# Kernel optimization log

Hardware: AMD Instinct MI355X
Metric: run time of the kernel (lower is better)

## Reference

```python
import jax, jax.numpy as jnp
import numpy as np

ANCHORS = [[(0.0156,0.0203),(0.025,0.0469),(0.0516,0.0359)],
           [(0.0469,0.0953),(0.0969,0.0703),(0.0922,0.1859)],
           [(0.1813,0.1406),(0.2438,0.3094),(0.5828,0.5094)]]
IMG = 640.0; NC = 80; NA = 3
LAM_NOOBJ = 1.0; LAM_OBJ = 1.0; LAM_CLS = 1.0; LAM_BOX = 5.0
ALPHA = 0.25; GAMMA = 2.0
GRIDS = [(80, 80), (40, 40), (20, 20)]


def _bce(x, t):
    # numerically-stable BCEWithLogits, reduction='none'
    return jnp.maximum(x, 0.0) - x * t + jnp.log1p(jnp.exp(-jnp.abs(x)))


def _focal(x, t):
    p = jax.nn.sigmoid(x)
    pt = p * t + (1.0 - p) * (1.0 - t)
    at = ALPHA * t + (1.0 - ALPHA) * (1.0 - t)
    return at * (1.0 - pt) ** GAMMA


def setup_inputs() -> dict:
    key = jax.random.key(0)
    ks = jax.random.split(key, 6)
    p0 = jax.random.normal(ks[0], (16, 255, 80, 80), jnp.float32)
    p1 = jax.random.normal(ks[1], (16, 255, 40, 40), jnp.float32)
    p2 = jax.random.normal(ks[2], (16, 255, 20, 20), jnp.float32)
    cxy = jax.random.uniform(ks[3], (16, 32, 2), jnp.float32, 32.0, 608.0)
    wh = jax.random.uniform(ks[4], (16, 32, 2), jnp.float32, 8.0, 256.0)
    target_boxes = jnp.clip(jnp.concatenate([cxy - wh / 2, cxy + wh / 2], -1), 0.0, IMG)
    target_labels = jax.random.randint(ks[5], (16, 32), 0, NC)
    return {"p0": p0, "p1": p1, "p2": p2, "target_boxes": target_boxes, "target_labels": target_labels}


def _loss(preds, boxes, labels):
    anchors = jnp.asarray(ANCHORS, jnp.float32)  # (3, 3, 2)
    B, N = labels.shape
    x1, y1, x2, y2 = boxes[..., 0], boxes[..., 1], boxes[..., 2], boxes[..., 3]
    bw = jnp.clip((x2 - x1) / IMG, 1e-6, 1.0)
    bh = jnp.clip((y2 - y1) / IMG, 1e-6, 1.0)
    # shape IoU against all 9 anchors -> top-1 (scale, anchor) per GT
    aw = anchors.reshape(-1, 2)  # (9, 2)
    inter = jnp.minimum(bw[..., None], aw[:, 0]) * jnp.minimum(bh[..., None], aw[:, 1])
    iou = inter / (bw[..., None] * bh[..., None] + aw[:, 0] * aw[:, 1] - inter + 1e-9)  # (B,N,9)
    best = jnp.argmax(iou, -1)
    scale_idx = best // NA
    anchor_idx = best % NA
    valid = (labels >= 0) & (labels < NC)
    cx = jnp.clip((x1 + x2) * 0.5 / IMG, 0.0, 1.0 - 1e-6)
    cy = jnp.clip((y1 + y2) * 0.5 / IMG, 0.0, 1.0 - 1e-6)
    oh = jax.nn.one_hot(labels, NC, dtype=jnp.float32)  # (B,N,NC)
    tb = jnp.stack([cx, cy, bw, bh], -1)  # (B,N,4) normalized cxcywh
    obj_loss = 0.0; cls_loss = 0.0; box_loss = 0.0; npos = 0.0
    for s, (pred, (h, w)) in enumerate(zip(preds, GRIDS)):
        pred = pred.reshape(B, NA, 5 + NC, h, w)
        gx = cx * w; gy = cy * h
        gi = jnp.clip(jnp.floor(gx), 0, w - 1).astype(jnp.int32)
        gj = jnp.clip(jnp.floor(gy), 0, h - 1).astype(jnp.int32)
        fx = gx - gi; fy = gy - gj
        base = valid & (scale_idx == s)
        ones = jnp.ones_like(fx, bool)
        cand = [(0, 0, ones), (-1, 0, fx < 0.5), (1, 0, fx >= 0.5), (0, -1, fy < 0.5), (0, 1, fy >= 0.5)]
        Ms, GIs, GJs = [], [], []
        for di, dj, keep in cand:
            ngi = gi + di; ngj = gj + dj
            inb = (ngi >= 0) & (ngi < w) & (ngj >= 0) & (ngj < h)
            Ms.append(base & keep & inb)
            GIs.append(jnp.clip(ngi, 0, w - 1))
            GJs.append(jnp.clip(ngj, 0, h - 1))
        M = jnp.stack(Ms); GI = jnp.stack(GIs); GJ = jnp.stack(GJs)  # (5,B,N)
        bidx = jnp.arange(B, dtype=jnp.int32)[None, :, None]
        aidx = jnp.broadcast_to(anchor_idx.astype(jnp.int32)[None], M.shape)
        flat = ((bidx * NA + aidx) * h + GJ) * w + GI  # (5,B,N) index into (B,NA,h,w)
        ncell = B * NA * h * w
        safe = jnp.where(M, flat, ncell)  # invalid -> dummy row
        pos = jax.lax.stop_gradient(
            jnp.zeros(ncell + 1).at[safe].max(M.astype(jnp.float32))[:ncell].reshape(B, NA, h, w))
        cls_t = jax.lax.stop_gradient(
            jnp.zeros((ncell + 1, NC)).at[safe].max(
                jnp.broadcast_to(oh[None], (5, B, N, NC)) * M[..., None].astype(jnp.float32)
            )[:ncell].reshape(B, NA, h, w, NC))
        box_t = jnp.zeros((ncell + 1, 4)).at[safe].set(
            jnp.broadcast_to(tb[None], (5, B, N, 4)))[:ncell].reshape(B, NA, h, w, 4)
        # decode (YOLOv5 parameterization), normalized coords
        sig = jax.nn.sigmoid
        pxy = 2.0 * sig(pred[:, :, :2]) - 0.5  # (B,NA,2,h,w)
        gxr = jnp.arange(w, dtype=jnp.float32)[None, None, None, :]
        gyr = jnp.arange(h, dtype=jnp.float32)[None, None, :, None]
        pcx = (gxr + pxy[:, :, 0]) / w
        pcy = (gyr + pxy[:, :, 1]) / h
        pwh = (2.0 * sig(pred[:, :, 2:4])) ** 2 * anchors[s][None, :, :, None, None]
        pw = pwh[:, :, 0]; ph = pwh[:, :, 1]
        tcx = box_t[..., 0]; tcy = box_t[..., 1]; tw = box_t[..., 2]; th = box_t[..., 3]
        px1, px2 = pcx - pw / 2, pcx + pw / 2; py1, py2 = pcy - ph / 2, pcy + ph / 2
        tx1, tx2 = tcx - tw / 2, tcx + tw / 2; ty1, ty2 = tcy - th / 2, tcy + th / 2
        iw = jnp.maximum(jnp.minimum(px2, tx2) - jnp.maximum(px1, tx1), 0.0)
        ih = jnp.maximum(jnp.minimum(py2, ty2) - jnp.maximum(py1, ty1), 0.0)
        it = iw * ih
        un = pw * ph + tw * th - it + 1e-9
        iouc = it / un
        enc = (jnp.maximum(px2, tx2) - jnp.minimum(px1, tx1)) * (jnp.maximum(py2, ty2) - jnp.minimum(py1, ty1)) + 1e-9
        giou = iouc - (enc - un) / enc
        l1 = jnp.abs(pcx - tcx) + jnp.abs(pcy - tcy) + jnp.abs(pw - tw) + jnp.abs(ph - th)
        box_loss = box_loss + (((1.0 - giou) + l1) * pos).sum()
        pcls = jnp.transpose(pred[:, :, 5:], (0, 1, 3, 4, 2))  # (B,NA,h,w,NC)
        cls_loss = cls_loss + (_bce(pcls, cls_t).sum(-1) * pos).sum()
        pobj = pred[:, :, 4]
        fb = _focal(pobj, pos) * _bce(pobj, pos)
        obj_loss = obj_loss + (fb * jnp.where(pos > 0, LAM_OBJ, LAM_NOOBJ)).mean()
        npos = npos + pos.sum()
    d = jnp.maximum(npos, 1.0)
    return obj_loss + LAM_CLS * cls_loss / d + LAM_BOX * box_loss / d


def reference(p0, p1, p2, target_boxes, target_labels):
    return _loss([p0, p1, p2], target_boxes, target_labels)
```

## Files before the change

kernel.cpp:

```cpp
#include <hip/hip_runtime.h>
#include <math.h>


#define IMGF 640.0f
#define NCLS 80
#define NAK 3
#define NB 16
#define NT 32
#define H0 80
#define H1 40
#define H2 20
#define NCELL0 (NB * NAK * H0 * H0)
#define NCELL1 (NB * NAK * H1 * H1)
#define NCELL2 (NB * NAK * H2 * H2)
#define NCELL_TOTAL (NCELL0 + NCELL1 + NCELL2)
#define MAXPOS 1536
#define NDENSE (NCELL_TOTAL / 4)
#define NDBLK ((NDENSE + 255) / 256)
#define POS_BLOCKS (MAXPOS * 64 / 256)
#define HSIZE 4096

__device__ __constant__ float c_anchors[9][2] = {
    {0.0156f, 0.0203f}, {0.025f, 0.0469f}, {0.0516f, 0.0359f},
    {0.0469f, 0.0953f}, {0.0969f, 0.0703f}, {0.0922f, 0.1859f},
    {0.1813f, 0.1406f}, {0.2438f, 0.3094f}, {0.5828f, 0.5094f}};

__device__ inline float sgm(float x) { return 1.f / (1.f + expf(-x)); }
__device__ inline float bcef(float x, float t) {
    return fmaxf(x, 0.f) - x * t + log1pf(expf(-fabsf(x)));
}
__device__ inline float focal_bce(float x, float t) {
    float p = sgm(x);
    float pt = p * t + (1.f - p) * (1.f - t);
    float at = 0.25f * t + 0.75f * (1.f - t);
    float omp = 1.f - pt;
    return at * omp * omp * bcef(x, t);
}

__global__ __launch_bounds__(512) void assign_kernel(
    const float* __restrict__ boxes, const int* __restrict__ labels,
    int4* __restrict__ list, int* __restrict__ countg, int* __restrict__ done) {
    __shared__ int hkey[HSIZE];
    __shared__ int hord[HSIZE];
    __shared__ unsigned htm[HSIZE];
    __shared__ int lcount;
    for (int i = threadIdx.x; i < HSIZE; i += 512) {
        hkey[i] = -1;
        hord[i] = -1;
        htm[i] = 0u;
    }
    if (threadIdx.x == 0) lcount = 0;
    __syncthreads();

    int t = threadIdx.x;
    int b = t >> 5;
    int n = t & 31;
    int lab = labels[t];
    if (lab >= 0 && lab < NCLS) {
        float x1 = boxes[4 * t + 0], y1 = boxes[4 * t + 1];
        float x2 = boxes[4 * t + 2], y2 = boxes[4 * t + 3];
        float bw = fminf(fmaxf((x2 - x1) / IMGF, 1e-6f), 1.0f);
        float bh = fminf(fmaxf((y2 - y1) / IMGF, 1e-6f), 1.0f);
        float area = bw * bh;
        float best = -1.0f;
        int bestk = 0;
#pragma unroll
        for (int k = 0; k < 9; k++) {
            float aw = c_anchors[k][0], ah = c_anchors[k][1];
            float inter = fminf(bw, aw) * fminf(bh, ah);
            float iou = inter / (area + aw * ah - inter + 1e-9f);
            if (iou > best) { best = iou; bestk = k; }
        }
        int s = bestk / 3, a = bestk - 3 * s;
        float cx = fminf(fmaxf((x1 + x2) * 0.5f / IMGF, 0.f), 1.f - 1e-6f);
        float cy = fminf(fmaxf((y1 + y2) * 0.5f / IMGF, 0.f), 1.f - 1e-6f);
        int hw = (s == 0) ? H0 : ((s == 1) ? H1 : H2);
        int basecell = (s == 0) ? 0 : ((s == 1) ? NCELL0 : (NCELL0 + NCELL1));
        float gx = cx * (float)hw, gy = cy * (float)hw;
        int gi = min(max((int)floorf(gx), 0), hw - 1);
        int gj = min(max((int)floorf(gy), 0), hw - 1);
        float fx = gx - (float)gi, fy = gy - (float)gj;
        const int dis[5] = {0, -1, 1, 0, 0};
        const int djs[5] = {0, 0, 0, -1, 1};
        bool keep[5];
        keep[0] = true;
        keep[1] = (fx < 0.5f);
        keep[2] = (fx >= 0.5f);
        keep[3] = (fy < 0.5f);
        keep[4] = (fy >= 0.5f);
#pragma unroll
        for (int c = 0; c < 5; c++) {
            if (!keep[c]) continue;
            int ngi = gi + dis[c], ngj = gj + djs[c];
            if (ngi < 0 || ngi >= hw || ngj < 0 || ngj >= hw) continue;
            int cell = basecell + ((b * NAK + a) * hw + ngj) * hw + ngi;
            unsigned h = ((unsigned)cell * 2654435761u) >> 20;
            while (true) {
                int old = atomicCAS(&hkey[h], -1, cell);
                if (old == -1 || old == cell) break;
                h = (h + 1) & (HSIZE - 1);
            }
            atomicMax(&hord[h], c * (NB * NT) + t);
            atomicOr(&htm[h], 1u << n);
        }
    }
    __syncthreads();
    for (int i = threadIdx.x; i < HSIZE; i += 512) {
        if (hkey[i] >= 0) {
            int p = atomicAdd(&lcount, 1);
            list[p] = make_int4(hkey[i], hord[i], (int)htm[i], 0);
        }
    }
    __syncthreads();
    if (threadIdx.x == 0) {
        *countg = lcount;
        *done = 0;
    }
}

template <int HWC>
__device__ inline float obj4(const float* __restrict__ p, int cis, float inv) {
    int q = cis / HWC;
    int off = cis - q * HWC;
    const float4 v =
        *reinterpret_cast<const float4*>(p + ((size_t)q * 85 + 4) * HWC + off);
    return (focal_bce(v.x, 0.f) + focal_bce(v.y, 0.f) + focal_bce(v.z, 0.f) +
            focal_bce(v.w, 0.f)) *
           inv;
}

__global__ __launch_bounds__(256) void dense_kernel(
    const float* __restrict__ p0, const float* __restrict__ p1,
    const float* __restrict__ p2, float* __restrict__ dpart) {
    int i = blockIdx.x * 256 + threadIdx.x;
    float obj = 0.f;
    if (i < NDENSE) {
        int c4 = i * 4;
        if (c4 < NCELL0)
            obj = obj4<H0 * H0>(p0, c4, 1.f / (float)NCELL0);
        else if (c4 < NCELL0 + NCELL1)
            obj = obj4<H1 * H1>(p1, c4 - NCELL0, 1.f / (float)NCELL1);
        else
            obj = obj4<H2 * H2>(p2, c4 - NCELL0 - NCELL1, 1.f / (float)NCELL2);
    }
#pragma unroll
    for (int off = 32; off > 0; off >>= 1) obj += __shfl_down(obj, off, 64);
    __shared__ float red[4];
    if ((threadIdx.x & 63) == 0) red[threadIdx.x >> 6] = obj;
    __syncthreads();
    if (threadIdx.x == 0)
        dpart[blockIdx.x] = red[0] + red[1] + red[2] + red[3];
}

__global__ __launch_bounds__(256) void pos_kernel(
    const float* __restrict__ p0, const float* __restrict__ p1,
    const float* __restrict__ p2, const float* __restrict__ boxes,
    const int* __restrict__ labels, const int4* __restrict__ list,
    const int* __restrict__ countg, int* __restrict__ done,
    const float* __restrict__ dpart, float* __restrict__ ppart,
    float* __restrict__ out) {
    int cnt = *countg;
    int w = (blockIdx.x * 256 + threadIdx.x) >> 6;
    int lane = threadIdx.x & 63;
    if (w < cnt) {
        int4 rec = list[w];
        int idx = rec.x;
        unsigned tm = (unsigned)rec.z;
        const float* p;
        int hw, s, base;
        float inv;
        if (idx < NCELL0) {
            p = p0; hw = H0; s = 0; base = 0; inv = 1.f / (float)NCELL0;
        } else if (idx < NCELL0 + NCELL1) {
            p = p1; hw = H1; s = 1; base = NCELL0; inv = 1.f / (float)NCELL1;
        } else {
            p = p2; hw = H2; s = 2; base = NCELL0 + NCELL1;
            inv = 1.f / (float)NCELL2;
        }
        int cell = idx - base;
        int x = cell % hw;
        int r = cell / hw;
        int y = r % hw;
        r /= hw;
        int a = r % NAK;
        int b = r / NAK;
        size_t HW = (size_t)hw * hw;
        const float* pc =
            p + (size_t)(b * 255 + a * 85) * HW + (size_t)y * hw + x;
        float cl = 0.f;
#pragma unroll
        for (int rep = 0; rep < 2; rep++) {
            int c = lane + 64 * rep;
            if (c < NCLS) {
                float tt = 0.f;
                unsigned tmp = tm;
                while (tmp) {
                    int n = __ffs(tmp) - 1;
                    tmp &= tmp - 1;
                    if (labels[(b << 5) + n] == c) tt = 1.f;
                }
                cl += bcef(pc[(size_t)(5 + c) * HW], tt);
            }
        }
#pragma unroll
        for (int off = 32; off > 0; off >>= 1) cl += __shfl_down(cl, off, 64);
        if (lane == 0) {
            float pobj = pc[4 * HW];
            float objc = (focal_bce(pobj, 1.f) - focal_bce(pobj, 0.f)) * inv;
            int wn = rec.y & (NB * NT - 1);
            float bx1 = boxes[4 * wn + 0], by1 = boxes[4 * wn + 1];
            float bx2 = boxes[4 * wn + 2], by2 = boxes[4 * wn + 3];
            float tw = fminf(fmaxf((bx2 - bx1) / IMGF, 1e-6f), 1.f);
            float th = fminf(fmaxf((by2 - by1) / IMGF, 1e-6f), 1.f);
            float tcx =
                fminf(fmaxf((bx1 + bx2) * 0.5f / IMGF, 0.f), 1.f - 1e-6f);
            float tcy =
                fminf(fmaxf((by1 + by2) * 0.5f / IMGF, 0.f), 1.f - 1e-6f);
            float l0 = pc[0], l1 = pc[HW], l2 = pc[2 * HW], l3 = pc[3 * HW];
            float pcx = ((float)x + 2.f * sgm(l0) - 0.5f) / (float)hw;
            float pcy = ((float)y + 2.f * sgm(l1) - 0.5f) / (float)hw;
            float sw = 2.f * sgm(l2), sh = 2.f * sgm(l3);
            float pw = sw * sw * c_anchors[s * 3 + a][0];
            float ph = sh * sh * c_anchors[s * 3 + a][1];
            float px1 = pcx - pw * 0.5f, px2 = pcx + pw * 0.5f;
            float py1 = pcy - ph * 0.5f, py2 = pcy + ph * 0.5f;
            float tx1 = tcx - tw * 0.5f, tx2 = tcx + tw * 0.5f;
            float ty1 = tcy - th * 0.5f, ty2 = tcy + th * 0.5f;
            float iw = fmaxf(fminf(px2, tx2) - fmaxf(px1, tx1), 0.f);
            float ih = fmaxf(fminf(py2, ty2) - fmaxf(py1, ty1), 0.f);
            float it = iw * ih;
            float un = pw * ph + tw * th - it + 1e-9f;
            float iou = it / un;
            float enc = (fmaxf(px2, tx2) - fminf(px1, tx1)) *
                            (fmaxf(py2, ty2) - fminf(py1, ty1)) +
                        1e-9f;
            float giou = iou - (enc - un) / enc;
            float l1l = fabsf(pcx - tcx) + fabsf(pcy - tcy) + fabsf(pw - tw) +
                        fabsf(ph - th);
            ppart[3 * w] = cl;
            ppart[3 * w + 1] = 1.f - giou + l1l;
            ppart[3 * w + 2] = objc;
        }
    }
    __shared__ int amLast;
    __syncthreads();
    if (threadIdx.x == 0) {
        __threadfence();
        int old = atomicAdd(done, 1);
        amLast = (old == POS_BLOCKS - 1) ? 1 : 0;
    }
    __syncthreads();
    if (amLast) {
        __threadfence();
        float obj = 0.f, cls = 0.f, box = 0.f;
        for (int i = threadIdx.x; i < NDBLK; i += 256) obj += dpart[i];
        for (int i = threadIdx.x; i < cnt; i += 256) {
            cls += ppart[3 * i];
            box += ppart[3 * i + 1];
            obj += ppart[3 * i + 2];
        }
#pragma unroll
        for (int off = 32; off > 0; off >>= 1) {
            obj += __shfl_down(obj, off, 64);
            cls += __shfl_down(cls, off, 64);
            box += __shfl_down(box, off, 64);
        }
        __shared__ float red[4][3];
        int wv = threadIdx.x >> 6;
        if ((threadIdx.x & 63) == 0) {
            red[wv][0] = obj;
            red[wv][1] = cls;
            red[wv][2] = box;
        }
        __syncthreads();
        if (threadIdx.x == 0) {
            float o = red[0][0] + red[1][0] + red[2][0] + red[3][0];
            float c = red[0][1] + red[1][1] + red[2][1] + red[3][1];
            float bx = red[0][2] + red[1][2] + red[2][2] + red[3][2];
            float d = fmaxf((float)cnt, 1.f);
            out[0] = o + (c + 5.f * bx) / d;
        }
    }
}

extern "C" void kernel_launch(void* const* d_in, const int* in_sizes, int n_in,
                              void* d_out, int out_size, void* d_ws,
                              size_t ws_size, hipStream_t stream) {
    const float* p0 = (const float*)d_in[0];
    const float* p1 = (const float*)d_in[1];
    const float* p2 = (const float*)d_in[2];
    const float* boxes = (const float*)d_in[3];
    const int* labels = (const int*)d_in[4];
    float* out = (float*)d_out;

    char* ws = (char*)d_ws;
    int4* list = (int4*)ws;
    size_t off = (size_t)MAXPOS * 16;
    int* countg = (int*)(ws + off);
    int* done = (int*)(ws + off + 4);
    off += 16;
    float* dpart = (float*)(ws + off);
    off += (size_t)((NDBLK + 3) / 4 * 4) * 4;
    float* ppart = (float*)(ws + off);

    assign_kernel<<<1, 512, 0, stream>>>(boxes, labels, list, countg, done);
    dense_kernel<<<NDBLK, 256, 0, stream>>>(p0, p1, p2, dpart);
    pos_kernel<<<POS_BLOCKS, 256, 0, stream>>>(p0, p1, p2, boxes, labels, list,
                                               countg, done, dpart, ppart, out);
}
```

Measured before the change: 31.19 us.

## Fuse assign, dense and positive kernels into one persistent kernel with flag sync

Merges the three launches into a single 384-block kernel. Block 0 builds the target-assignment hash list and then publishes it through a global ready flag. Every block runs a grid-stride dense objectness reduction, then spins on the flag before processing positive cells, and the last block does the final reduction. This removes two kernel launch gaps and lets the assignment overlap the dense pass. In exchange it depends on all blocks being co-resident to avoid deadlock, carries 48KB of shared memory in every block, and relies on resetting the flag for the next call.

```diff
diff --git a/kernel.cpp b/kernel.cpp
--- a/kernel.cpp
+++ b/kernel.cpp
@@ -16,9 +16,9 @@
 #define NCELL_TOTAL (NCELL0 + NCELL1 + NCELL2)
 #define MAXPOS 1536
 #define NDENSE (NCELL_TOTAL / 4)
-#define NDBLK ((NDENSE + 255) / 256)
-#define POS_BLOCKS (MAXPOS * 64 / 256)
+#define NBLOCKS 384
 #define HSIZE 4096
+#define READY_MAGIC 0x5A17C0DEu
 
 __device__ __constant__ float c_anchors[9][2] = {
     {0.0156f, 0.0203f}, {0.025f, 0.0469f}, {0.0516f, 0.0359f},
@@ -35,87 +35,6 @@
     float at = 0.25f * t + 0.75f * (1.f - t);
     float omp = 1.f - pt;
     return at * omp * omp * bcef(x, t);
-}
-
-__global__ __launch_bounds__(512) void assign_kernel(
-    const float* __restrict__ boxes, const int* __restrict__ labels,
-    int4* __restrict__ list, int* __restrict__ countg, int* __restrict__ done) {
-    __shared__ int hkey[HSIZE];
-    __shared__ int hord[HSIZE];
-    __shared__ unsigned htm[HSIZE];
-    __shared__ int lcount;
-    for (int i = threadIdx.x; i < HSIZE; i += 512) {
-        hkey[i] = -1;
-        hord[i] = -1;
-        htm[i] = 0u;
-    }
-    if (threadIdx.x == 0) lcount = 0;
-    __syncthreads();
-
-    int t = threadIdx.x;
-    int b = t >> 5;
-    int n = t & 31;
-    int lab = labels[t];
-    if (lab >= 0 && lab < NCLS) {
-        float x1 = boxes[4 * t + 0], y1 = boxes[4 * t + 1];
-        float x2 = boxes[4 * t + 2], y2 = boxes[4 * t + 3];
-        float bw = fminf(fmaxf((x2 - x1) / IMGF, 1e-6f), 1.0f);
-        float bh = fminf(fmaxf((y2 - y1) / IMGF, 1e-6f), 1.0f);
-        float area = bw * bh;
-        float best = -1.0f;
-        int bestk = 0;
-#pragma unroll
-        for (int k = 0; k < 9; k++) {
-            float aw = c_anchors[k][0], ah = c_anchors[k][1];
-            float inter = fminf(bw, aw) * fminf(bh, ah);
-            float iou = inter / (area + aw * ah - inter + 1e-9f);
-            if (iou > best) { best = iou; bestk = k; }
-        }
-        int s = bestk / 3, a = bestk - 3 * s;
-        float cx = fminf(fmaxf((x1 + x2) * 0.5f / IMGF, 0.f), 1.f - 1e-6f);
-        float cy = fminf(fmaxf((y1 + y2) * 0.5f / IMGF, 0.f), 1.f - 1e-6f);
-        int hw = (s == 0) ? H0 : ((s == 1) ? H1 : H2);
-        int basecell = (s == 0) ? 0 : ((s == 1) ? NCELL0 : (NCELL0 + NCELL1));
-        float gx = cx * (float)hw, gy = cy * (float)hw;
-        int gi = min(max((int)floorf(gx), 0), hw - 1);
-        int gj = min(max((int)floorf(gy), 0), hw - 1);
-        float fx = gx - (float)gi, fy = gy - (float)gj;
-        const int dis[5] = {0, -1, 1, 0, 0};
-        const int djs[5] = {0, 0, 0, -1, 1};
-        bool keep[5];
-        keep[0] = true;
-        keep[1] = (fx < 0.5f);
-        keep[2] = (fx >= 0.5f);
-        keep[3] = (fy < 0.5f);
-        keep[4] = (fy >= 0.5f);
-#pragma unroll
-        for (int c = 0; c < 5; c++) {
-            if (!keep[c]) continue;
-            int ngi = gi + dis[c], ngj = gj + djs[c];
-            if (ngi < 0 || ngi >= hw || ngj < 0 || ngj >= hw) continue;
-            int cell = basecell + ((b * NAK + a) * hw + ngj) * hw + ngi;
-            unsigned h = ((unsigned)cell * 2654435761u) >> 20;
-            while (true) {
-                int old = atomicCAS(&hkey[h], -1, cell);
-                if (old == -1 || old == cell) break;
-                h = (h + 1) & (HSIZE - 1);
-            }
-            atomicMax(&hord[h], c * (NB * NT) + t);
-            atomicOr(&htm[h], 1u << n);
-        }
-    }
-    __syncthreads();
-    for (int i = threadIdx.x; i < HSIZE; i += 512) {
-        if (hkey[i] >= 0) {
-            int p = atomicAdd(&lcount, 1);
-            list[p] = make_int4(hkey[i], hord[i], (int)htm[i], 0);
-        }
-    }
-    __syncthreads();
-    if (threadIdx.x == 0) {
-        *countg = lcount;
-        *done = 0;
-    }
 }
 
 template <int HWC>
@@ -129,38 +48,132 @@
            inv;
 }
 
-__global__ __launch_bounds__(256) void dense_kernel(
+__global__ __launch_bounds__(256, 2) void yolo_fused(
     const float* __restrict__ p0, const float* __restrict__ p1,
-    const float* __restrict__ p2, float* __restrict__ dpart) {
-    int i = blockIdx.x * 256 + threadIdx.x;
+    const float* __restrict__ p2, const float* __restrict__ boxes,
+    const int* __restrict__ labels, int4* __restrict__ list,
+    int* __restrict__ countg, unsigned* __restrict__ flag,
+    int* __restrict__ done, float* __restrict__ dpart,
+    float* __restrict__ ppart, float* __restrict__ out) {
+    __shared__ int hkey[HSIZE];
+    __shared__ int hord[HSIZE];
+    __shared__ unsigned htm[HSIZE];
+    __shared__ int lcount;
+    __shared__ float redd[4];
+    __shared__ float redf[4][3];
+    __shared__ int amLast;
+
+    if (blockIdx.x == 0) {
+        for (int i = threadIdx.x; i < HSIZE; i += 256) {
+            hkey[i] = -1;
+            hord[i] = -1;
+            htm[i] = 0u;
+        }
+        if (threadIdx.x == 0) lcount = 0;
+        __syncthreads();
+        for (int half = 0; half < 2; half++) {
+            int t = threadIdx.x + (half << 8);
+            int b = t >> 5;
+            int n = t & 31;
+            int lab = labels[t];
+            if (lab >= 0 && lab < NCLS) {
+                float x1 = boxes[4 * t + 0], y1 = boxes[4 * t + 1];
+                float x2 = boxes[4 * t + 2], y2 = boxes[4 * t + 3];
+                float bw = fminf(fmaxf((x2 - x1) / IMGF, 1e-6f), 1.0f);
+                float bh = fminf(fmaxf((y2 - y1) / IMGF, 1e-6f), 1.0f);
+                float area = bw * bh;
+                float best = -1.0f;
+                int bestk = 0;
+#pragma unroll
+                for (int k = 0; k < 9; k++) {
+                    float aw = c_anchors[k][0], ah = c_anchors[k][1];
+                    float inter = fminf(bw, aw) * fminf(bh, ah);
+                    float iou = inter / (area + aw * ah - inter + 1e-9f);
+                    if (iou > best) { best = iou; bestk = k; }
+                }
+                int s = bestk / 3, a = bestk - 3 * s;
+                float cx =
+                    fminf(fmaxf((x1 + x2) * 0.5f / IMGF, 0.f), 1.f - 1e-6f);
+                float cy =
+                    fminf(fmaxf((y1 + y2) * 0.5f / IMGF, 0.f), 1.f - 1e-6f);
+                int hw = (s == 0) ? H0 : ((s == 1) ? H1 : H2);
+                int basecell =
+                    (s == 0) ? 0 : ((s == 1) ? NCELL0 : (NCELL0 + NCELL1));
+                float gx = cx * (float)hw, gy = cy * (float)hw;
+                int gi = min(max((int)floorf(gx), 0), hw - 1);
+                int gj = min(max((int)floorf(gy), 0), hw - 1);
+                float fx = gx - (float)gi, fy = gy - (float)gj;
+                const int dis[5] = {0, -1, 1, 0, 0};
+                const int djs[5] = {0, 0, 0, -1, 1};
+                bool keep[5];
+                keep[0] = true;
+                keep[1] = (fx < 0.5f);
+                keep[2] = (fx >= 0.5f);
+                keep[3] = (fy < 0.5f);
+                keep[4] = (fy >= 0.5f);
+#pragma unroll
+                for (int c = 0; c < 5; c++) {
+                    if (!keep[c]) continue;
+                    int ngi = gi + dis[c], ngj = gj + djs[c];
+                    if (ngi < 0 || ngi >= hw || ngj < 0 || ngj >= hw) continue;
+                    int cell = basecell + ((b * NAK + a) * hw + ngj) * hw + ngi;
+                    unsigned h = ((unsigned)cell * 2654435761u) >> 20;
+                    while (true) {
+                        int old = atomicCAS(&hkey[h], -1, cell);
+                        if (old == -1 || old == cell) break;
+                        h = (h + 1) & (HSIZE - 1);
+                    }
+                    atomicMax(&hord[h], c * (NB * NT) + t);
+                    atomicOr(&htm[h], 1u << n);
+                }
+            }
+        }
+        __syncthreads();
+        for (int i = threadIdx.x; i < HSIZE; i += 256) {
+            if (hkey[i] >= 0) {
+                int p = atomicAdd(&lcount, 1);
+                list[p] = make_int4(hkey[i], hord[i], (int)htm[i], 0);
+            }
+        }
+        __syncthreads();
+        if (threadIdx.x == 0) {
+            *countg = lcount;
+            *done = 0;
+            __threadfence();
+            __hip_atomic_store(flag, READY_MAGIC, __ATOMIC_RELAXED,
+                               __HIP_MEMORY_SCOPE_AGENT);
+        }
+    }
+
     float obj = 0.f;
-    if (i < NDENSE) {
+    for (int i = blockIdx.x * 256 + threadIdx.x; i < NDENSE;
+         i += NBLOCKS * 256) {
         int c4 = i * 4;
         if (c4 < NCELL0)
-            obj = obj4<H0 * H0>(p0, c4, 1.f / (float)NCELL0);
+            obj += obj4<H0 * H0>(p0, c4, 1.f / (float)NCELL0);
         else if (c4 < NCELL0 + NCELL1)
-            obj = obj4<H1 * H1>(p1, c4 - NCELL0, 1.f / (float)NCELL1);
+            obj += obj4<H1 * H1>(p1, c4 - NCELL0, 1.f / (float)NCELL1);
         else
-            obj = obj4<H2 * H2>(p2, c4 - NCELL0 - NCELL1, 1.f / (float)NCELL2);
+            obj +=
+                obj4<H2 * H2>(p2, c4 - NCELL0 - NCELL1, 1.f / (float)NCELL2);
     }
 #pragma unroll
     for (int off = 32; off > 0; off >>= 1) obj += __shfl_down(obj, off, 64);
-    __shared__ float red[4];
-    if ((threadIdx.x & 63) == 0) red[threadIdx.x >> 6] = obj;
+    if ((threadIdx.x & 63) == 0) redd[threadIdx.x >> 6] = obj;
     __syncthreads();
     if (threadIdx.x == 0)
-        dpart[blockIdx.x] = red[0] + red[1] + red[2] + red[3];
-}
-
-__global__ __launch_bounds__(256) void pos_kernel(
-    const float* __restrict__ p0, const float* __restrict__ p1,
-    const float* __restrict__ p2, const float* __restrict__ boxes,
-    const int* __restrict__ labels, const int4* __restrict__ list,
-    const int* __restrict__ countg, int* __restrict__ done,
-    const float* __restrict__ dpart, float* __restrict__ ppart,
-    float* __restrict__ out) {
+        dpart[blockIdx.x] = redd[0] + redd[1] + redd[2] + redd[3];
+
+    if (threadIdx.x == 0) {
+        while (__hip_atomic_load(flag, __ATOMIC_RELAXED,
+                                 __HIP_MEMORY_SCOPE_AGENT) != READY_MAGIC)
+            __builtin_amdgcn_s_sleep(1);
+    }
+    __syncthreads();
+    __threadfence();
     int cnt = *countg;
-    int w = (blockIdx.x * 256 + threadIdx.x) >> 6;
+
+    int w = blockIdx.x * 4 + (threadIdx.x >> 6);
     int lane = threadIdx.x & 63;
     if (w < cnt) {
         int4 rec = list[w];
@@ -242,43 +255,42 @@
             ppart[3 * w + 2] = objc;
         }
     }
-    __shared__ int amLast;
+
     __syncthreads();
     if (threadIdx.x == 0) {
         __threadfence();
-        int old = atomicAdd(done, 1);
-        amLast = (old == POS_BLOCKS - 1) ? 1 : 0;
+        amLast = (atomicAdd(done, 1) == NBLOCKS - 1) ? 1 : 0;
     }
     __syncthreads();
     if (amLast) {
         __threadfence();
-        float obj = 0.f, cls = 0.f, box = 0.f;
-        for (int i = threadIdx.x; i < NDBLK; i += 256) obj += dpart[i];
+        float o = 0.f, cls = 0.f, box = 0.f;
+        for (int i = threadIdx.x; i < NBLOCKS; i += 256) o += dpart[i];
         for (int i = threadIdx.x; i < cnt; i += 256) {
             cls += ppart[3 * i];
             box += ppart[3 * i + 1];
-            obj += ppart[3 * i + 2];
+            o += ppart[3 * i + 2];
         }
 #pragma unroll
         for (int off = 32; off > 0; off >>= 1) {
-            obj += __shfl_down(obj, off, 64);
+            o += __shfl_down(o, off, 64);
             cls += __shfl_down(cls, off, 64);
             box += __shfl_down(box, off, 64);
         }
-        __shared__ float red[4][3];
         int wv = threadIdx.x >> 6;
         if ((threadIdx.x & 63) == 0) {
-            red[wv][0] = obj;
-            red[wv][1] = cls;
-            red[wv][2] = box;
+            redf[wv][0] = o;
+            redf[wv][1] = cls;
+            redf[wv][2] = box;
         }
         __syncthreads();
         if (threadIdx.x == 0) {
-            float o = red[0][0] + red[1][0] + red[2][0] + red[3][0];
-            float c = red[0][1] + red[1][1] + red[2][1] + red[3][1];
-            float bx = red[0][2] + red[1][2] + red[2][2] + red[3][2];
+            float oo = redf[0][0] + redf[1][0] + redf[2][0] + redf[3][0];
+            float cc = redf[0][1] + redf[1][1] + redf[2][1] + redf[3][1];
+            float bb = redf[0][2] + redf[1][2] + redf[2][2] + redf[3][2];
             float d = fmaxf((float)cnt, 1.f);
-            out[0] = o + (c + 5.f * bx) / d;
+            out[0] = oo + (cc + 5.f * bb) / d;
+            *flag = 0u;
         }
     }
 }
@@ -297,14 +309,14 @@
     int4* list = (int4*)ws;
     size_t off = (size_t)MAXPOS * 16;
     int* countg = (int*)(ws + off);
-    int* done = (int*)(ws + off + 4);
+    unsigned* flag = (unsigned*)(ws + off + 4);
+    int* done = (int*)(ws + off + 8);
     off += 16;
     float* dpart = (float*)(ws + off);
-    off += (size_t)((NDBLK + 3) / 4 * 4) * 4;
+    off += (size_t)NBLOCKS * 4;
     float* ppart = (float*)(ws + off);
 
-    assign_kernel<<<1, 512, 0, stream>>>(boxes, labels, list, countg, done);
-    dense_kernel<<<NDBLK, 256, 0, stream>>>(p0, p1, p2, dpart);
-    pos_kernel<<<POS_BLOCKS, 256, 0, stream>>>(p0, p1, p2, boxes, labels, list,
-                                               countg, done, dpart, ppart, out);
-}
+    yolo_fused<<<NBLOCKS, 256, 0, stream>>>(p0, p1, p2, boxes, labels, list,
+                                            countg, flag, done, dpart, ppart,
+                                            out);
+}
```

After: 52.67 us. 1.69x slower.

## Fuse assignment, dense objectness and positive-cell loss into one kernel

Applied to the files above, without the earlier changes.

Replaces the three-kernel pipeline (single-block assign, dense objectness, positive-cell kernel with a last-block reduction) with one 384-block kernel plus a tiny finalize kernel. Every block redundantly rebuilds the GT-to-cell hash table in shared memory, issuing its two float4 objectness loads before doing so to hide latency, then handles the positive cells whose key modulo the block count equals its block id. This removes the serial single-block assign launch and the global list handoff. In exchange every block repeats the 512-target assignment and shared-memory atomics, and the hash table shrinks to 2048 entries.

```diff
diff --git a/kernel.cpp b/kernel.cpp
--- a/kernel.cpp
+++ b/kernel.cpp
@@ -16,9 +16,8 @@
 #define NCELL_TOTAL (NCELL0 + NCELL1 + NCELL2)
 #define MAXPOS 1536
 #define NDENSE (NCELL_TOTAL / 4)
-#define NDBLK ((NDENSE + 255) / 256)
-#define POS_BLOCKS (MAXPOS * 64 / 256)
-#define HSIZE 4096
+#define NBLKF 384
+#define HSIZE 2048
 
 __device__ __constant__ float c_anchors[9][2] = {
     {0.0156f, 0.0203f}, {0.025f, 0.0469f}, {0.0516f, 0.0359f},
@@ -37,135 +36,143 @@
     return at * omp * omp * bcef(x, t);
 }
 
-__global__ __launch_bounds__(512) void assign_kernel(
-    const float* __restrict__ boxes, const int* __restrict__ labels,
-    int4* __restrict__ list, int* __restrict__ countg, int* __restrict__ done) {
+__device__ inline const float* objaddr(const float* __restrict__ p0,
+                                       const float* __restrict__ p1,
+                                       const float* __restrict__ p2, int c4,
+                                       float& inv) {
+    if (c4 < NCELL0) {
+        inv = 1.f / (float)NCELL0;
+        int q = c4 / (H0 * H0);
+        return p0 + ((size_t)q * 85 + 4) * (H0 * H0) + (c4 - q * (H0 * H0));
+    } else if (c4 < NCELL0 + NCELL1) {
+        inv = 1.f / (float)NCELL1;
+        c4 -= NCELL0;
+        int q = c4 / (H1 * H1);
+        return p1 + ((size_t)q * 85 + 4) * (H1 * H1) + (c4 - q * (H1 * H1));
+    } else {
+        inv = 1.f / (float)NCELL2;
+        c4 -= NCELL0 + NCELL1;
+        int q = c4 / (H2 * H2);
+        return p2 + ((size_t)q * 85 + 4) * (H2 * H2) + (c4 - q * (H2 * H2));
+    }
+}
+
+__device__ inline float fb4_zero(float4 v) {
+    return focal_bce(v.x, 0.f) + focal_bce(v.y, 0.f) + focal_bce(v.z, 0.f) +
+           focal_bce(v.w, 0.f);
+}
+
+__global__ __launch_bounds__(256) void yolo_main(
+    const float* __restrict__ p0, const float* __restrict__ p1,
+    const float* __restrict__ p2, const float* __restrict__ boxes,
+    const int* __restrict__ labels, float* __restrict__ dpart) {
     __shared__ int hkey[HSIZE];
     __shared__ int hord[HSIZE];
     __shared__ unsigned htm[HSIZE];
-    __shared__ int lcount;
-    for (int i = threadIdx.x; i < HSIZE; i += 512) {
+    __shared__ int qslots[MAXPOS];
+    __shared__ int qn;
+    __shared__ float redf[4][4];
+
+    const int tid = threadIdx.x;
+    const int bid = blockIdx.x;
+
+    int i0 = bid * 256 + tid;
+    int i1 = i0 + NBLKF * 256;
+    float inv0, inv1 = 0.f;
+    const float4 v0 =
+        *reinterpret_cast<const float4*>(objaddr(p0, p1, p2, i0 * 4, inv0));
+    float4 v1 = make_float4(0.f, 0.f, 0.f, 0.f);
+    const bool has1 = (i1 < NDENSE);
+    if (has1)
+        v1 = *reinterpret_cast<const float4*>(
+            objaddr(p0, p1, p2, i1 * 4, inv1));
+
+    for (int i = tid; i < HSIZE; i += 256) {
         hkey[i] = -1;
         hord[i] = -1;
         htm[i] = 0u;
     }
-    if (threadIdx.x == 0) lcount = 0;
-    __syncthreads();
-
-    int t = threadIdx.x;
-    int b = t >> 5;
-    int n = t & 31;
-    int lab = labels[t];
-    if (lab >= 0 && lab < NCLS) {
-        float x1 = boxes[4 * t + 0], y1 = boxes[4 * t + 1];
-        float x2 = boxes[4 * t + 2], y2 = boxes[4 * t + 3];
-        float bw = fminf(fmaxf((x2 - x1) / IMGF, 1e-6f), 1.0f);
-        float bh = fminf(fmaxf((y2 - y1) / IMGF, 1e-6f), 1.0f);
-        float area = bw * bh;
-        float best = -1.0f;
-        int bestk = 0;
-#pragma unroll
-        for (int k = 0; k < 9; k++) {
-            float aw = c_anchors[k][0], ah = c_anchors[k][1];
-            float inter = fminf(bw, aw) * fminf(bh, ah);
-            float iou = inter / (area + aw * ah - inter + 1e-9f);
-            if (iou > best) { best = iou; bestk = k; }
-        }
-        int s = bestk / 3, a = bestk - 3 * s;
-        float cx = fminf(fmaxf((x1 + x2) * 0.5f / IMGF, 0.f), 1.f - 1e-6f);
-        float cy = fminf(fmaxf((y1 + y2) * 0.5f / IMGF, 0.f), 1.f - 1e-6f);
-        int hw = (s == 0) ? H0 : ((s == 1) ? H1 : H2);
-        int basecell = (s == 0) ? 0 : ((s == 1) ? NCELL0 : (NCELL0 + NCELL1));
-        float gx = cx * (float)hw, gy = cy * (float)hw;
-        int gi = min(max((int)floorf(gx), 0), hw - 1);
-        int gj = min(max((int)floorf(gy), 0), hw - 1);
-        float fx = gx - (float)gi, fy = gy - (float)gj;
-        const int dis[5] = {0, -1, 1, 0, 0};
-        const int djs[5] = {0, 0, 0, -1, 1};
-        bool keep[5];
-        keep[0] = true;
-        keep[1] = (fx < 0.5f);
-        keep[2] = (fx >= 0.5f);
-        keep[3] = (fy < 0.5f);
-        keep[4] = (fy >= 0.5f);
-#pragma unroll
-        for (int c = 0; c < 5; c++) {
-            if (!keep[c]) continue;
-            int ngi = gi + dis[c], ngj = gj + djs[c];
-            if (ngi < 0 || ngi >= hw || ngj < 0 || ngj >= hw) continue;
-            int cell = basecell + ((b * NAK + a) * hw + ngj) * hw + ngi;
-            unsigned h = ((unsigned)cell * 2654435761u) >> 20;
-            while (true) {
-                int old = atomicCAS(&hkey[h], -1, cell);
-                if (old == -1 || old == cell) break;
-                h = (h + 1) & (HSIZE - 1);
+    if (tid == 0) qn = 0;
+    __syncthreads();
+    for (int half = 0; half < 2; half++) {
+        int t = tid + (half << 8);
+        int b = t >> 5;
+        int n = t & 31;
+        int lab = labels[t];
+        if (lab >= 0 && lab < NCLS) {
+            float x1 = boxes[4 * t + 0], y1 = boxes[4 * t + 1];
+            float x2 = boxes[4 * t + 2], y2 = boxes[4 * t + 3];
+            float bw = fminf(fmaxf((x2 - x1) / IMGF, 1e-6f), 1.0f);
+            float bh = fminf(fmaxf((y2 - y1) / IMGF, 1e-6f), 1.0f);
+            float area = bw * bh;
+            float best = -1.0f;
+            int bestk = 0;
+#pragma unroll
+            for (int k = 0; k < 9; k++) {
+                float aw = c_anchors[k][0], ah = c_anchors[k][1];
+                float inter = fminf(bw, aw) * fminf(bh, ah);
+                float iou = inter / (area + aw * ah - inter + 1e-9f);
+                if (iou > best) { best = iou; bestk = k; }
             }
-            atomicMax(&hord[h], c * (NB * NT) + t);
-            atomicOr(&htm[h], 1u << n);
-        }
-    }
-    __syncthreads();
-    for (int i = threadIdx.x; i < HSIZE; i += 512) {
-        if (hkey[i] >= 0) {
-            int p = atomicAdd(&lcount, 1);
-            list[p] = make_int4(hkey[i], hord[i], (int)htm[i], 0);
-        }
-    }
-    __syncthreads();
-    if (threadIdx.x == 0) {
-        *countg = lcount;
-        *done = 0;
-    }
-}
-
-template <int HWC>
-__device__ inline float obj4(const float* __restrict__ p, int cis, float inv) {
-    int q = cis / HWC;
-    int off = cis - q * HWC;
-    const float4 v =
-        *reinterpret_cast<const float4*>(p + ((size_t)q * 85 + 4) * HWC + off);
-    return (focal_bce(v.x, 0.f) + focal_bce(v.y, 0.f) + focal_bce(v.z, 0.f) +
-            focal_bce(v.w, 0.f)) *
-           inv;
-}
-
-__global__ __launch_bounds__(256) void dense_kernel(
-    const float* __restrict__ p0, const float* __restrict__ p1,
-    const float* __restrict__ p2, float* __restrict__ dpart) {
-    int i = blockIdx.x * 256 + threadIdx.x;
-    float obj = 0.f;
-    if (i < NDENSE) {
-        int c4 = i * 4;
-        if (c4 < NCELL0)
-            obj = obj4<H0 * H0>(p0, c4, 1.f / (float)NCELL0);
-        else if (c4 < NCELL0 + NCELL1)
-            obj = obj4<H1 * H1>(p1, c4 - NCELL0, 1.f / (float)NCELL1);
-        else
-            obj = obj4<H2 * H2>(p2, c4 - NCELL0 - NCELL1, 1.f / (float)NCELL2);
-    }
-#pragma unroll
-    for (int off = 32; off > 0; off >>= 1) obj += __shfl_down(obj, off, 64);
-    __shared__ float red[4];
-    if ((threadIdx.x & 63) == 0) red[threadIdx.x >> 6] = obj;
-    __syncthreads();
-    if (threadIdx.x == 0)
-        dpart[blockIdx.x] = red[0] + red[1] + red[2] + red[3];
-}
-
-__global__ __launch_bounds__(256) void pos_kernel(
-    const float* __restrict__ p0, const float* __restrict__ p1,
-    const float* __restrict__ p2, const float* __restrict__ boxes,
-    const int* __restrict__ labels, const int4* __restrict__ list,
-    const int* __restrict__ countg, int* __restrict__ done,
-    const float* __restrict__ dpart, float* __restrict__ ppart,
-    float* __restrict__ out) {
-    int cnt = *countg;
-    int w = (blockIdx.x * 256 + threadIdx.x) >> 6;
-    int lane = threadIdx.x & 63;
-    if (w < cnt) {
-        int4 rec = list[w];
-        int idx = rec.x;
-        unsigned tm = (unsigned)rec.z;
+            int s = bestk / 3, a = bestk - 3 * s;
+            float cx = fminf(fmaxf((x1 + x2) * 0.5f / IMGF, 0.f), 1.f - 1e-6f);
+            float cy = fminf(fmaxf((y1 + y2) * 0.5f / IMGF, 0.f), 1.f - 1e-6f);
+            int hw = (s == 0) ? H0 : ((s == 1) ? H1 : H2);
+            int basecell =
+                (s == 0) ? 0 : ((s == 1) ? NCELL0 : (NCELL0 + NCELL1));
+            float gx = cx * (float)hw, gy = cy * (float)hw;
+            int gi = min(max((int)floorf(gx), 0), hw - 1);
+            int gj = min(max((int)floorf(gy), 0), hw - 1);
+            float fx = gx - (float)gi, fy = gy - (float)gj;
+            const int dis[5] = {0, -1, 1, 0, 0};
+            const int djs[5] = {0, 0, 0, -1, 1};
+            bool keep[5];
+            keep[0] = true;
+            keep[1] = (fx < 0.5f);
+            keep[2] = (fx >= 0.5f);
+            keep[3] = (fy < 0.5f);
+            keep[4] = (fy >= 0.5f);
+#pragma unroll
+            for (int c = 0; c < 5; c++) {
+                if (!keep[c]) continue;
+                int ngi = gi + dis[c], ngj = gj + djs[c];
+                if (ngi < 0 || ngi >= hw || ngj < 0 || ngj >= hw) continue;
+                int cell = basecell + ((b * NAK + a) * hw + ngj) * hw + ngi;
+                unsigned h = ((unsigned)cell * 2654435761u) >> 21;
+                while (true) {
+                    int old = atomicCAS(&hkey[h], -1, cell);
+                    if (old == -1 || old == cell) break;
+                    h = (h + 1) & (HSIZE - 1);
+                }
+                atomicMax(&hord[h], c * (NB * NT) + t);
+                atomicOr(&htm[h], 1u << n);
+            }
+        }
+    }
+    __syncthreads();
+
+    for (int i = tid; i < HSIZE; i += 256) {
+        int k = hkey[i];
+        if (k >= 0 && (k % NBLKF) == bid) {
+            int p = atomicAdd(&qn, 1);
+            qslots[p] = i;
+        }
+    }
+
+    float obj_c = fb4_zero(v0) * inv0;
+    if (has1) obj_c += fb4_zero(v1) * inv1;
+
+    __syncthreads();
+    const int nq = qn;
+
+    const int wv = tid >> 6;
+    const int lane = tid & 63;
+    float cls_a = 0.f, box_a = 0.f, objc_a = 0.f;
+    for (int qi = wv; qi < nq; qi += 4) {
+        int slot = qslots[qi];
+        int idx = hkey[slot];
+        unsigned tm = htm[slot];
+        int ord = hord[slot];
         const float* p;
         int hw, s, base;
         float inv;
@@ -205,9 +212,10 @@
 #pragma unroll
         for (int off = 32; off > 0; off >>= 1) cl += __shfl_down(cl, off, 64);
         if (lane == 0) {
+            cls_a += cl;
             float pobj = pc[4 * HW];
-            float objc = (focal_bce(pobj, 1.f) - focal_bce(pobj, 0.f)) * inv;
-            int wn = rec.y & (NB * NT - 1);
+            objc_a += (focal_bce(pobj, 1.f) - focal_bce(pobj, 0.f)) * inv;
+            int wn = ord & (NB * NT - 1);
             float bx1 = boxes[4 * wn + 0], by1 = boxes[4 * wn + 1];
             float bx2 = boxes[4 * wn + 2], by2 = boxes[4 * wn + 3];
             float tw = fminf(fmaxf((bx2 - bx1) / IMGF, 1e-6f), 1.f);
@@ -237,49 +245,65 @@
             float giou = iou - (enc - un) / enc;
             float l1l = fabsf(pcx - tcx) + fabsf(pcy - tcy) + fabsf(pw - tw) +
                         fabsf(ph - th);
-            ppart[3 * w] = cl;
-            ppart[3 * w + 1] = 1.f - giou + l1l;
-            ppart[3 * w + 2] = objc;
-        }
-    }
-    __shared__ int amLast;
+            box_a += 1.f - giou + l1l;
+        }
+    }
+
+    float s_obj = obj_c + objc_a;
+#pragma unroll
+    for (int off = 32; off > 0; off >>= 1) {
+        s_obj += __shfl_down(s_obj, off, 64);
+        cls_a += __shfl_down(cls_a, off, 64);
+        box_a += __shfl_down(box_a, off, 64);
+    }
+    if (lane == 0) {
+        redf[wv][0] = s_obj;
+        redf[wv][1] = cls_a;
+        redf[wv][2] = box_a;
+    }
+    __syncthreads();
+    if (tid == 0) {
+        float* dst = dpart + (size_t)bid * 4;
+        dst[0] = redf[0][0] + redf[1][0] + redf[2][0] + redf[3][0];
+        dst[1] = redf[0][1] + redf[1][1] + redf[2][1] + redf[3][1];
+        dst[2] = redf[0][2] + redf[1][2] + redf[2][2] + redf[3][2];
+        dst[3] = (float)nq;
+    }
+}
+
+__global__ __launch_bounds__(256) void yolo_finalize(
+    const float* __restrict__ dpart, float* __restrict__ out) {
+    float o = 0.f, cls = 0.f, box = 0.f, np = 0.f;
+    for (int i = threadIdx.x; i < NBLKF; i += 256) {
+        const float* src = dpart + (size_t)i * 4;
+        o += src[0];
+        cls += src[1];
+        box += src[2];
+        np += src[3];
+    }
+#pragma unroll
+    for (int off = 32; off > 0; off >>= 1) {
+        o += __shfl_down(o, off, 64);
+        cls += __shfl_down(cls, off, 64);
+        box += __shfl_down(box, off, 64);
+        np += __shfl_down(np, off, 64);
+    }
+    __shared__ float red[4][4];
+    int wv = threadIdx.x >> 6;
+    if ((threadIdx.x & 63) == 0) {
+        red[wv][0] = o;
+        red[wv][1] = cls;
+        red[wv][2] = box;
+        red[wv][3] = np;
+    }
     __syncthreads();
     if (threadIdx.x == 0) {
-        __threadfence();
-        int old = atomicAdd(done, 1);
-        amLast = (old == POS_BLOCKS - 1) ? 1 : 0;
-    }
-    __syncthreads();
-    if (amLast) {
-        __threadfence();
-        float obj = 0.f, cls = 0.f, box = 0.f;
-        for (int i = threadIdx.x; i < NDBLK; i += 256) obj += dpart[i];
-        for (int i = threadIdx.x; i < cnt; i += 256) {
-            cls += ppart[3 * i];
-            box += ppart[3 * i + 1];
-            obj += ppart[3 * i + 2];
-        }
-#pragma unroll
-        for (int off = 32; off > 0; off >>= 1) {
-            obj += __shfl_down(obj, off, 64);
-            cls += __shfl_down(cls, off, 64);
-            box += __shfl_down(box, off, 64);
-        }
-        __shared__ float red[4][3];
-        int wv = threadIdx.x >> 6;
-        if ((threadIdx.x & 63) == 0) {
-            red[wv][0] = obj;
-            red[wv][1] = cls;
-            red[wv][2] = box;
-        }
-        __syncthreads();
-        if (threadIdx.x == 0) {
-            float o = red[0][0] + red[1][0] + red[2][0] + red[3][0];
-            float c = red[0][1] + red[1][1] + red[2][1] + red[3][1];
-            float bx = red[0][2] + red[1][2] + red[2][2] + red[3][2];
-            float d = fmaxf((float)cnt, 1.f);
-            out[0] = o + (c + 5.f * bx) / d;
-        }
+        float oo = red[0][0] + red[1][0] + red[2][0] + red[3][0];
+        float cc = red[0][1] + red[1][1] + red[2][1] + red[3][1];
+        float bb = red[0][2] + red[1][2] + red[2][2] + red[3][2];
+        float nn = red[0][3] + red[1][3] + red[2][3] + red[3][3];
+        float d = fmaxf(nn, 1.f);
+        out[0] = oo + (cc + 5.f * bb) / d;
     }
 }
 
@@ -293,18 +317,8 @@
     const int* labels = (const int*)d_in[4];
     float* out = (float*)d_out;
 
-    char* ws = (char*)d_ws;
-    int4* list = (int4*)ws;
-    size_t off = (size_t)MAXPOS * 16;
-    int* countg = (int*)(ws + off);
-    int* done = (int*)(ws + off + 4);
-    off += 16;
-    float* dpart = (float*)(ws + off);
-    off += (size_t)((NDBLK + 3) / 4 * 4) * 4;
-    float* ppart = (float*)(ws + off);
-
-    assign_kernel<<<1, 512, 0, stream>>>(boxes, labels, list, countg, done);
-    dense_kernel<<<NDBLK, 256, 0, stream>>>(p0, p1, p2, dpart);
-    pos_kernel<<<POS_BLOCKS, 256, 0, stream>>>(p0, p1, p2, boxes, labels, list,
-                                               countg, done, dpart, ppart, out);
-}
+    float* dpart = (float*)d_ws;
+
+    yolo_main<<<NBLKF, 256, 0, stream>>>(p0, p1, p2, boxes, labels, dpart);
+    yolo_finalize<<<1, 256, 0, stream>>>(dpart, out);
+}
```

New measurement: 34.13 us. +9.4%, slower.
